# Kernel tuning notes

Hardware: AMD Instinct MI355X
Metric: run time of the kernel (lower is better)

Reference implementation:

```python
import jax, jax.numpy as jnp
import numpy as np
from jax import lax

WINDOW_SIZE = 11
SIGMA = 1.5
CHANNELS = 3
C1 = 0.01 ** 2
C2 = 0.03 ** 2


def _create_window():
    coords = jnp.arange(WINDOW_SIZE, dtype=jnp.float32) - WINDOW_SIZE // 2
    g = jnp.exp(-coords ** 2 / (2.0 * SIGMA ** 2))
    g = g / g.sum()
    w2d = g[:, None] * g[None, :]                      # (11, 11)
    # depthwise kernel, OIHW with groups=channels -> (C, 1, k, k)
    return jnp.broadcast_to(w2d, (CHANNELS, 1, WINDOW_SIZE, WINDOW_SIZE))


def _dwconv(x, window):
    pad = WINDOW_SIZE // 2
    return lax.conv_general_dilated(
        x, window,
        window_strides=(1, 1),
        padding=[(pad, pad), (pad, pad)],
        dimension_numbers=('NCHW', 'OIHW', 'NCHW'),
        feature_group_count=CHANNELS,
    )


def setup_inputs() -> dict:
    key = jax.random.key(0)
    k1, k2 = jax.random.split(key)
    pred = jax.random.uniform(k1, (32, 3, 512, 512), dtype=jnp.float32)
    target = jax.random.uniform(k2, (32, 3, 512, 512), dtype=jnp.float32)
    return {"pred": pred, "target": target}


def reference(pred, target):
    pred = pred.astype(jnp.float32)
    target = target.astype(jnp.float32)
    window = _create_window()

    mu1 = _dwconv(pred, window)
    mu2 = _dwconv(target, window)
    mu1_sq = mu1 * mu1
    mu2_sq = mu2 * mu2
    mu1_mu2 = mu1 * mu2
    sigma1_sq = _dwconv(pred * pred, window) - mu1_sq
    sigma2_sq = _dwconv(target * target, window) - mu2_sq
    sigma12 = _dwconv(pred * target, window) - mu1_mu2

    ssim_map = ((2.0 * mu1_mu2 + C1) * (2.0 * sigma12 + C2)) / (
        (mu1_sq + mu2_sq + C1) * (sigma1_sq + sigma2_sq + C2))
    return 1.0 - ssim_map.mean()
```

## Files before the change

### kernel.cpp

```cpp
#include <hip/hip_runtime.h>
#include <hip/hip_bf16.h>
#include <math.h>

#define BLOCK 256
#define IMG 512
#define SW 88
#define RSTR 40
#define NBLOCKS 3072
#define NACC 128
#define N_TOTAL 25165824.0f

typedef float f32x4 __attribute__((ext_vector_type(4)));
typedef short s16x8 __attribute__((ext_vector_type(8)));

struct WB { unsigned short b[11]; float c2; float k1; float k2; };
union FR { unsigned int u[4]; s16x8 s; };

__device__ __forceinline__ unsigned int pk2(float a, float b) {
    union { __hip_bfloat162 h; unsigned int u; } cv;
    cv.h = __float22bfloat162_rn(make_float2(a, b));
    return cv.u;
}

__device__ __forceinline__ void stage5(unsigned short (*sq)[16][SW],
                                       int r, int i, float4 xv, float4 yv) {
    *(uint2*)&sq[0][r][4*i] = make_uint2(pk2(xv.x,xv.y), pk2(xv.z,xv.w));
    *(uint2*)&sq[1][r][4*i] = make_uint2(pk2(yv.x,yv.y), pk2(yv.z,yv.w));
    *(uint2*)&sq[2][r][4*i] = make_uint2(pk2(xv.x*xv.x,xv.y*xv.y), pk2(xv.z*xv.z,xv.w*xv.w));
    *(uint2*)&sq[3][r][4*i] = make_uint2(pk2(yv.x*yv.x,yv.y*yv.y), pk2(yv.z*yv.z,yv.w*yv.w));
    *(uint2*)&sq[4][r][4*i] = make_uint2(pk2(xv.x*yv.x,xv.y*yv.y), pk2(xv.z*yv.z,xv.w*yv.w));
}

__device__ __forceinline__ void load_set(const float* __restrict__ P,
                                         const float* __restrict__ T,
                                         int R0, int step,
                                         int rA, int colA, bool okcA,
                                         bool hasB, int rB, int colB, bool okcB,
                                         float4& xA, float4& yA, float4& xB, float4& yB) {
    const int gr = R0 - 5 + 16 * step + rA;
    if (okcA && gr >= 0 && gr < IMG) {
        xA = *(const float4*)(P + ((size_t)gr << 9) + colA);
        yA = *(const float4*)(T + ((size_t)gr << 9) + colA);
    } else { xA = make_float4(0,0,0,0); yA = make_float4(0,0,0,0); }
    const int grB = R0 - 5 + 16 * step + rB;
    if (hasB && okcB && grB >= 0 && grB < IMG) {
        xB = *(const float4*)(P + ((size_t)grB << 9) + colB);
        yB = *(const float4*)(T + ((size_t)grB << 9) + colB);
    } else { xB = make_float4(0,0,0,0); yB = make_float4(0,0,0,0); }
}

__global__ __launch_bounds__(BLOCK, 4)
void ssim_tiled(const float* __restrict__ pred,
                const float* __restrict__ targ,
                float* __restrict__ accum, WB wb) {
    __shared__ unsigned short s_q[5][16][SW];
    __shared__ unsigned short s_ring[5][64][RSTR];

    const int tid = threadIdx.x;
    const int bx    = blockIdx.x;
    const int plane = bx >> 5;
    const int rem   = bx & 31;
    const int tx    = rem >> 2;
    const int ry    = rem & 3;
    const int C0    = tx * 64;
    const int R0    = ry * 128;

    const float* P = pred + (size_t)plane * (IMG * IMG);
    const float* T = targ + (size_t)plane * (IMG * IMG);

    const int w    = tid >> 6;
    const int lane = tid & 63;
    const int l15  = lane & 15;
    const int quad = lane >> 4;

    const int slotA = w * 80 + lane;
    const int rA = slotA / 20, iA = slotA % 20;
    const int colA = C0 - 8 + 4 * iA;
    const bool okcA = (colA >= 0) && (colA + 4 <= IMG);
    const bool hasB = (lane < 16);
    const int slotB = w * 80 + 64 + l15;
    const int rB = slotB / 20, iB = slotB % 20;
    const int colB = C0 - 8 + 4 * iB;
    const bool okcB = (colB >= 0) && (colB + 4 <= IMG);

    const float c2 = wb.c2, K1 = wb.k1, K2 = wb.k2;
    const f32x4 z = {0.f, 0.f, 0.f, 0.f};
    float lsum = 0.f;

    float4 pxA, pyA, pxB, pyB;
    load_set(P, T, R0, 0, rA, colA, okcA, hasB, rB, colB, okcB, pxA, pyA, pxB, pyB);
    float4 sxA[2], syA[2], sxB[2], syB[2];
    load_set(P, T, R0, 1, rA, colA, okcA, hasB, rB, colB, okcB,
             sxA[1], syA[1], sxB[1], syB[1]);

    FR bw, aw0, aw1;
    {
        const int ti = lane & 31;
        int tv = 0;
#pragma unroll
        for (int k = 0; k < 11; ++k) tv = (ti == k) ? (int)wb.b[k] : tv;
        const int tnext = __shfl(tv, (lane + 1) & 63);
        const int pairT = (tv & 0xffff) | (tnext << 16);
        const int base_b = 8 * quad - l15 - 3;
        const int base0  = 8 * quad - l15;
        const int base1  = 8 * quad - l15 - 16;
#pragma unroll
        for (int t = 0; t < 4; ++t) {
            bw.u[t]  = (unsigned int)__shfl(pairT, (base_b + 2 * t) & 63);
            aw0.u[t] = (unsigned int)__shfl(pairT, (base0 + 2 * t) & 63);
            aw1.u[t] = (unsigned int)__shfl(pairT, (base1 + 2 * t) & 63);
        }
    }

    stage5(s_q, rA, iA, pxA, pyA);
    if (hasB) stage5(s_q, rB, iB, pxB, pyB);
    __syncthreads();

    const int rcol = 16 * w + l15;

#pragma unroll
    for (int s = 0; s < 9; ++s) {
        if (s < 7) {
            load_set(P, T, R0, s + 2, rA, colA, okcA, hasB, rB, colB, okcB,
                     sxA[s & 1], syA[s & 1], sxB[s & 1], syB[s & 1]);
        }

        {
            FR a0, a1, a2, a3, a4;
            a0.s = *(const s16x8*)&s_q[0][l15][16*w + 8*quad];
            a1.s = *(const s16x8*)&s_q[1][l15][16*w + 8*quad];
            a2.s = *(const s16x8*)&s_q[2][l15][16*w + 8*quad];
            a3.s = *(const s16x8*)&s_q[3][l15][16*w + 8*quad];
            a4.s = *(const s16x8*)&s_q[4][l15][16*w + 8*quad];
            f32x4 d0 = __builtin_amdgcn_mfma_f32_16x16x32_bf16(a0.s, bw.s, z, 0, 0, 0);
            f32x4 d1 = __builtin_amdgcn_mfma_f32_16x16x32_bf16(a1.s, bw.s, z, 0, 0, 0);
            f32x4 d2 = __builtin_amdgcn_mfma_f32_16x16x32_bf16(a2.s, bw.s, z, 0, 0, 0);
            f32x4 d3 = __builtin_amdgcn_mfma_f32_16x16x32_bf16(a3.s, bw.s, z, 0, 0, 0);
            f32x4 d4 = __builtin_amdgcn_mfma_f32_16x16x32_bf16(a4.s, bw.s, z, 0, 0, 0);
            const int pb = (16 * s + 4 * quad) & 31;
            *(uint2*)&s_ring[0][rcol][pb] = make_uint2(pk2(d0[0],d0[1]), pk2(d0[2],d0[3]));
            *(uint2*)&s_ring[1][rcol][pb] = make_uint2(pk2(d1[0],d1[1]), pk2(d1[2],d1[3]));
            *(uint2*)&s_ring[2][rcol][pb] = make_uint2(pk2(d2[0],d2[1]), pk2(d2[2],d2[3]));
            *(uint2*)&s_ring[3][rcol][pb] = make_uint2(pk2(d3[0],d3[1]), pk2(d3[2],d3[3]));
            *(uint2*)&s_ring[4][rcol][pb] = make_uint2(pk2(d4[0],d4[1]), pk2(d4[2],d4[3]));
        }

        if (s >= 1) {
            const FR aw = ((s - 1) & 1) ? aw1 : aw0;
            f32x4 acc[5];
#pragma unroll
            for (int q = 0; q < 5; ++q) {
                FR b; b.s = *(const s16x8*)&s_ring[q][rcol][quad * 8];
                acc[q] = __builtin_amdgcn_mfma_f32_16x16x32_bf16(aw.s, b.s, z, 0, 0, 0);
            }
#pragma unroll
            for (int i = 0; i < 4; ++i) {
                const float u1  = acc[0][i];
                const float u2  = acc[1][i];
                const float m11 = u1 * u1;
                const float m22 = u2 * u2;
                const float m12 = u1 * u2;
                const float e11 = acc[2][i] * c2;
                const float e22 = acc[3][i] * c2;
                const float e12 = acc[4][i] * c2;
                const float A = fmaf(2.f, m12, K1);
                const float B = fmaf(2.f, e12 - m12, K2);
                const float C = m11 + m22 + K1;
                const float D = (e11 + e22) - (m11 + m22) + K2;
                lsum = fmaf(A * B, __builtin_amdgcn_rcpf(C * D), lsum);
            }
        }

        __syncthreads();

        if (s < 8) {
            stage5(s_q, rA, iA, sxA[(s + 1) & 1], syA[(s + 1) & 1]);
            if (hasB) stage5(s_q, rB, iB, sxB[(s + 1) & 1], syB[(s + 1) & 1]);
            __syncthreads();
        }
    }

#pragma unroll
    for (int off = 32; off > 0; off >>= 1) lsum += __shfl_down(lsum, off, 64);
    if (lane == 0) atomicAdd(&accum[(bx * 4 + w) & (NACC - 1)], lsum);
}

__global__ void ssim_finalize(const float* __restrict__ accum, float* __restrict__ out) {
    const int l = threadIdx.x;
    float v = accum[l] + accum[l + 64];
#pragma unroll
    for (int off = 32; off > 0; off >>= 1) v += __shfl_down(v, off, 64);
    if (l == 0) out[0] = 1.0f - v * (1.0f / N_TOTAL);
}

extern "C" void kernel_launch(void* const* d_in, const int* in_sizes, int n_in,
                              void* d_out, int out_size, void* d_ws, size_t ws_size,
                              hipStream_t stream) {
    const float* pred = (const float*)d_in[0];
    const float* targ = (const float*)d_in[1];
    float* out = (float*)d_out;
    float* ws  = (float*)d_ws;

    WB wb;
    {
        double gg[11], sum = 0.0;
        for (int k = 0; k < 11; ++k) {
            const double d = (double)(k - 5);
            gg[k] = exp(-d * d / 4.5);
            sum += gg[k];
        }
        double sbf = 0.0;
        for (int k = 0; k < 11; ++k) {
            union { float f; unsigned int u; } cv;
            cv.f = (float)(gg[k] / sum);
            const unsigned int r = (cv.u + 0x7fffu + ((cv.u >> 16) & 1u)) >> 16;
            wb.b[k] = (unsigned short)r;
            union { float f; unsigned int u; } bk;
            bk.u = r << 16;
            sbf += (double)bk.f;
        }
        const double s2 = sbf * sbf;
        wb.c2 = (float)s2;
        wb.k1 = (float)(0.0001 * s2 * s2);
        wb.k2 = (float)(0.0009 * s2 * s2);
    }

    hipMemsetAsync(ws, 0, NACC * sizeof(float), stream);
    ssim_tiled<<<NBLOCKS, BLOCK, 0, stream>>>(pred, targ, ws, wb);
    ssim_finalize<<<1, 64, 0, stream>>>(ws, out);
}
```

Baseline: 244.8 us.

## Keep horizontal-pass MFMA outputs in registers and feed vertical pass via 16x16x16 MFMAs

Removes the shared-memory ring buffer between the horizontal and vertical Gaussian MFMA passes. The packed bf16 results stay in a two-slot register array, and the vertical pass becomes two chained 16x16x16 bf16 MFMAs that combine the current and previous row blocks. Barrier placement is reordered so the next tile is staged into shared memory before the vertical pass, with a lighter lgkmcnt-plus-s_barrier sync, and the occupancy hint goes from 4 to 7 blocks. This cuts LDS traffic and LDS footprint, at the cost of more registers held live and twice as many (smaller) MFMA issues in the vertical pass.

```diff
diff --git a/kernel.cpp b/kernel.cpp
--- a/kernel.cpp
+++ b/kernel.cpp
@@ -5,16 +5,34 @@
 #define BLOCK 256
 #define IMG 512
 #define SW 88
-#define RSTR 40
 #define NBLOCKS 3072
 #define NACC 128
 #define N_TOTAL 25165824.0f
 
 typedef float f32x4 __attribute__((ext_vector_type(4)));
 typedef short s16x8 __attribute__((ext_vector_type(8)));
+typedef short s16x4 __attribute__((ext_vector_type(4)));
 
 struct WB { unsigned short b[11]; float c2; float k1; float k2; };
-union FR { unsigned int u[4]; s16x8 s; };
+union FR  { unsigned int u[4]; s16x8 s; };
+union FR2 { unsigned int u[2]; s16x4 s; };
+
+#if __has_builtin(__builtin_amdgcn_mfma_f32_16x16x16bf16_1k)
+#define MFMA16(A,B,C) __builtin_amdgcn_mfma_f32_16x16x16bf16_1k((A),(B),(C),0,0,0)
+#else
+__device__ __forceinline__ f32x4 mfma16_asm(s16x4 a, s16x4 b, f32x4 c) {
+    f32x4 d;
+    asm("v_mfma_f32_16x16x16_bf16 %0, %1, %2, %3" : "=v"(d) : "v"(a), "v"(b), "v"(c));
+    return d;
+}
+#define MFMA16(A,B,C) mfma16_asm((A),(B),(C))
+#endif
+
+#define WG_SYNC() do { \
+    asm volatile("s_waitcnt lgkmcnt(0)" ::: "memory"); \
+    __builtin_amdgcn_s_barrier(); \
+    asm volatile("" ::: "memory"); \
+} while (0)
 
 __device__ __forceinline__ unsigned int pk2(float a, float b) {
     union { __hip_bfloat162 h; unsigned int u; } cv;
@@ -49,12 +67,11 @@
     } else { xB = make_float4(0,0,0,0); yB = make_float4(0,0,0,0); }
 }
 
-__global__ __launch_bounds__(BLOCK, 4)
+__global__ __launch_bounds__(BLOCK, 7)
 void ssim_tiled(const float* __restrict__ pred,
                 const float* __restrict__ targ,
                 float* __restrict__ accum, WB wb) {
     __shared__ unsigned short s_q[5][16][SW];
-    __shared__ unsigned short s_ring[5][64][RSTR];
 
     const int tid = threadIdx.x;
     const int bx    = blockIdx.x;
@@ -93,7 +110,7 @@
     load_set(P, T, R0, 1, rA, colA, okcA, hasB, rB, colB, okcB,
              sxA[1], syA[1], sxB[1], syB[1]);
 
-    FR bw, aw0, aw1;
+    FR bw; FR2 awlo, awhi;
     {
         const int ti = lane & 31;
         int tv = 0;
@@ -102,21 +119,23 @@
         const int tnext = __shfl(tv, (lane + 1) & 63);
         const int pairT = (tv & 0xffff) | (tnext << 16);
         const int base_b = 8 * quad - l15 - 3;
-        const int base0  = 8 * quad - l15;
-        const int base1  = 8 * quad - l15 - 16;
-#pragma unroll
-        for (int t = 0; t < 4; ++t) {
-            bw.u[t]  = (unsigned int)__shfl(pairT, (base_b + 2 * t) & 63);
-            aw0.u[t] = (unsigned int)__shfl(pairT, (base0 + 2 * t) & 63);
-            aw1.u[t] = (unsigned int)__shfl(pairT, (base1 + 2 * t) & 63);
+        const int baseL  = 4 * quad - l15;
+        const int baseH  = 4 * quad - l15 + 16;
+#pragma unroll
+        for (int t = 0; t < 4; ++t)
+            bw.u[t] = (unsigned int)__shfl(pairT, (base_b + 2 * t) & 63);
+#pragma unroll
+        for (int t = 0; t < 2; ++t) {
+            awlo.u[t] = (unsigned int)__shfl(pairT, (baseL + 2 * t) & 63);
+            awhi.u[t] = (unsigned int)__shfl(pairT, (baseH + 2 * t) & 63);
         }
     }
 
     stage5(s_q, rA, iA, pxA, pyA);
     if (hasB) stage5(s_q, rB, iB, pxB, pyB);
-    __syncthreads();
-
-    const int rcol = 16 * w + l15;
+    WG_SYNC();
+
+    FR2 vb[2][5];
 
 #pragma unroll
     for (int s = 0; s < 9; ++s) {
@@ -137,32 +156,38 @@
             f32x4 d2 = __builtin_amdgcn_mfma_f32_16x16x32_bf16(a2.s, bw.s, z, 0, 0, 0);
             f32x4 d3 = __builtin_amdgcn_mfma_f32_16x16x32_bf16(a3.s, bw.s, z, 0, 0, 0);
             f32x4 d4 = __builtin_amdgcn_mfma_f32_16x16x32_bf16(a4.s, bw.s, z, 0, 0, 0);
-            const int pb = (16 * s + 4 * quad) & 31;
-            *(uint2*)&s_ring[0][rcol][pb] = make_uint2(pk2(d0[0],d0[1]), pk2(d0[2],d0[3]));
-            *(uint2*)&s_ring[1][rcol][pb] = make_uint2(pk2(d1[0],d1[1]), pk2(d1[2],d1[3]));
-            *(uint2*)&s_ring[2][rcol][pb] = make_uint2(pk2(d2[0],d2[1]), pk2(d2[2],d2[3]));
-            *(uint2*)&s_ring[3][rcol][pb] = make_uint2(pk2(d3[0],d3[1]), pk2(d3[2],d3[3]));
-            *(uint2*)&s_ring[4][rcol][pb] = make_uint2(pk2(d4[0],d4[1]), pk2(d4[2],d4[3]));
+            vb[s & 1][0].u[0] = pk2(d0[0], d0[1]); vb[s & 1][0].u[1] = pk2(d0[2], d0[3]);
+            vb[s & 1][1].u[0] = pk2(d1[0], d1[1]); vb[s & 1][1].u[1] = pk2(d1[2], d1[3]);
+            vb[s & 1][2].u[0] = pk2(d2[0], d2[1]); vb[s & 1][2].u[1] = pk2(d2[2], d2[3]);
+            vb[s & 1][3].u[0] = pk2(d3[0], d3[1]); vb[s & 1][3].u[1] = pk2(d3[2], d3[3]);
+            vb[s & 1][4].u[0] = pk2(d4[0], d4[1]); vb[s & 1][4].u[1] = pk2(d4[2], d4[3]);
+        }
+
+        WG_SYNC();
+
+        if (s < 8) {
+            stage5(s_q, rA, iA, sxA[(s + 1) & 1], syA[(s + 1) & 1]);
+            if (hasB) stage5(s_q, rB, iB, sxB[(s + 1) & 1], syB[(s + 1) & 1]);
         }
 
         if (s >= 1) {
-            const FR aw = ((s - 1) & 1) ? aw1 : aw0;
-            f32x4 acc[5];
-#pragma unroll
-            for (int q = 0; q < 5; ++q) {
-                FR b; b.s = *(const s16x8*)&s_ring[q][rcol][quad * 8];
-                acc[q] = __builtin_amdgcn_mfma_f32_16x16x32_bf16(aw.s, b.s, z, 0, 0, 0);
-            }
+            f32x4 acc5[5];
+#pragma unroll
+            for (int q = 0; q < 5; ++q)
+                acc5[q] = MFMA16(awhi.s, vb[s & 1][q].s, z);
+#pragma unroll
+            for (int q = 0; q < 5; ++q)
+                acc5[q] = MFMA16(awlo.s, vb[1 - (s & 1)][q].s, acc5[q]);
 #pragma unroll
             for (int i = 0; i < 4; ++i) {
-                const float u1  = acc[0][i];
-                const float u2  = acc[1][i];
+                const float u1  = acc5[0][i];
+                const float u2  = acc5[1][i];
                 const float m11 = u1 * u1;
                 const float m22 = u2 * u2;
                 const float m12 = u1 * u2;
-                const float e11 = acc[2][i] * c2;
-                const float e22 = acc[3][i] * c2;
-                const float e12 = acc[4][i] * c2;
+                const float e11 = acc5[2][i] * c2;
+                const float e22 = acc5[3][i] * c2;
+                const float e12 = acc5[4][i] * c2;
                 const float A = fmaf(2.f, m12, K1);
                 const float B = fmaf(2.f, e12 - m12, K2);
                 const float C = m11 + m22 + K1;
@@ -171,13 +196,7 @@
             }
         }
 
-        __syncthreads();
-
-        if (s < 8) {
-            stage5(s_q, rA, iA, sxA[(s + 1) & 1], syA[(s + 1) & 1]);
-            if (hasB) stage5(s_q, rB, iB, sxB[(s + 1) & 1], syB[(s + 1) & 1]);
-            __syncthreads();
-        }
+        if (s < 8) WG_SYNC();
     }
 
 #pragma unroll
```

After: 480.6 us. 96.3% more time.
